# Kernel optimization log

Measured on AMD Instinct MI355X. Metric: run time of the kernel, lower is better.

Reference implementation:

```python
import jax, jax.numpy as jnp
import numpy as np

B, L, C, H = 1, 256, 128, 4  # batch, seq len, c_z, n_heads
D = C // H                    # head_dim = 32


def setup_inputs() -> dict:
    key = jax.random.key(0)
    ks = jax.random.split(key, 8)
    w = lambda k, shape: jax.random.normal(k, shape, jnp.float32) * 0.02
    return {
        "pair": jax.random.normal(ks[0], (B, L, L, C), jnp.float32),
        "ln_g": jnp.ones((C,), jnp.float32),
        "ln_b": jnp.zeros((C,), jnp.float32),
        "Wq": w(ks[1], (C, C)),
        "Wk": w(ks[2], (C, C)),
        "Wv": w(ks[3], (C, C)),
        "Wbias": w(ks[4], (C, H)),
        "Wo": w(ks[5], (C, C)),
        "bo": jnp.zeros((C,), jnp.float32),
        "Wg": w(ks[6], (C, C)),
        "bg": jnp.zeros((C,), jnp.float32),
    }


def reference(pair, ln_g, ln_b, Wq, Wk, Wv, Wbias, Wo, bo, Wg, bg):
    # mode == 'starting': no transpose of pair
    # LayerNorm over c_z
    mu = jnp.mean(pair, axis=-1, keepdims=True)
    var = jnp.mean(jnp.square(pair - mu), axis=-1, keepdims=True)
    z = (pair - mu) * jax.lax.rsqrt(var + 1e-5) * ln_g + ln_b

    q = (z @ Wq).reshape(B, L, L, H, D)
    k = (z @ Wk).reshape(B, L, L, H, D)
    v = (z @ Wv).reshape(B, L, L, H, D)

    # logits: [B, H, i, j, k], scaled by 1/sqrt(head_dim)
    attn = jnp.einsum('bijhd,bikhd->bhijk', q, k) * (1.0 / np.sqrt(D).astype(np.float32))
    # pairwise additive bias: bias_proj(z) -> [B, L, L, H] -> [B, H, 1, j, k]
    bias = jnp.einsum('bjkc,ch->bhjk', z, Wbias)[:, :, None, :, :]
    attn = jax.nn.softmax(attn + bias, axis=-1)

    out = jnp.einsum('bhijk,bikhd->bijhd', attn, v).reshape(B, L, L, C)
    result = pair + jax.nn.sigmoid(pair @ Wg + bg) * (out @ Wo + bo)
    return result
```

## Files before the change

kernel.cpp:

```cpp
#include <hip/hip_runtime.h>
#include <cstdint>
#include <cstddef>

#define L_ 256
#define C_ 128
#define H_ 4
#define D_ 32
#define NP_ (L_ * L_)

typedef unsigned short u16;
typedef uint32_t u32;
typedef __attribute__((ext_vector_type(8))) short bf16x8;
typedef __attribute__((ext_vector_type(4))) float f32x4;

__device__ __forceinline__ float bflo(u32 u) { union { u32 i; float f; } v; v.i = u << 16; return v.f; }
__device__ __forceinline__ float bfhi(u32 u) { union { u32 i; float f; } v; v.i = u & 0xffff0000u; return v.f; }
__device__ __forceinline__ float b2f(u16 u) { union { u32 i; float f; } v; v.i = ((u32)u) << 16; return v.f; }
__device__ __forceinline__ u16 f2b(float f) {
    u32 x = __float_as_uint(f);
    return (u16)((x + 0x7fffu + ((x >> 16) & 1u)) >> 16);
}
__device__ __forceinline__ u32 pk2(float lo, float hi) {
    return ((u32)f2b(hi) << 16) | (u32)f2b(lo);
}
__device__ __forceinline__ bf16x8 pack8(float4 a, float4 b) {
    union { u32 u[4]; bf16x8 v; } r;
    r.u[0] = pk2(a.x, a.y); r.u[1] = pk2(a.z, a.w);
    r.u[2] = pk2(b.x, b.y); r.u[3] = pk2(b.z, b.w);
    return r.v;
}

__global__ __launch_bounds__(256) void k_prep(
    const float* __restrict__ Wq, const float* __restrict__ Wk, const float* __restrict__ Wv,
    const float* __restrict__ Wo, const float* __restrict__ Wg,
    const float* __restrict__ Wbias, u16* __restrict__ Wt, float* __restrict__ WbT)
{
    __shared__ float tile[64][65];
    const int b = blockIdx.x, t = threadIdx.x;
    if (b < 20) {
        const int mat = b >> 2, tl = b & 3, tr = tl >> 1, tc = tl & 1;
        const float* W = (mat == 0) ? Wq : (mat == 1) ? Wk : (mat == 2) ? Wv : (mat == 3) ? Wo : Wg;
        const float s = (mat == 0) ? 0.2550680544705824f : 1.f;
        const int rlo = t >> 6, col = t & 63;
        #pragma unroll
        for (int m = 0; m < 16; ++m) {
            int row = m * 4 + rlo;
            tile[row][col] = W[(size_t)(tr * 64 + row) * C_ + tc * 64 + col];
        }
        __syncthreads();
        #pragma unroll
        for (int m = 0; m < 16; ++m) {
            int n = tc * 64 + m * 4 + rlo;
            int c = tr * 64 + col;
            Wt[mat * 16384 + n * C_ + c] = f2b(tile[col][m * 4 + rlo] * s);
        }
    } else {
        #pragma unroll
        for (int m = 0; m < 2; ++m) {
            int idx = m * 256 + t;
            int h = idx >> 7, c = idx & 127;
            WbT[h * C_ + c] = Wbias[c * H_ + h] * 1.4426950408889634f;
        }
    }
}

__global__ __launch_bounds__(256) void k_lnmm(
    const float* __restrict__ pair, const float* __restrict__ ln_g, const float* __restrict__ ln_b,
    const u16* __restrict__ Wt, const float* __restrict__ WbT,
    u16* __restrict__ qh, u16* __restrict__ kh, u16* __restrict__ vh,
    u16* __restrict__ biasN)
{
    __shared__ u16 zsh[64][136];

    const int t  = threadIdx.x;
    const int p0 = blockIdx.x * 64;
    const int row = t >> 2, seg = t & 3;

    float4 xv[8];
    float sum = 0.f, ss = 0.f;
    #pragma unroll
    for (int i = 0; i < 8; ++i) {
        int c = (seg + 4 * i) * 4;
        float4 x = *(const float4*)(pair + (size_t)(p0 + row) * C_ + c);
        xv[i] = x;
        sum += x.x + x.y + x.z + x.w;
        ss  += x.x * x.x + x.y * x.y + x.z * x.z + x.w * x.w;
    }
    sum += __shfl_xor(sum, 1); sum += __shfl_xor(sum, 2);
    ss  += __shfl_xor(ss, 1);  ss  += __shfl_xor(ss, 2);
    float mu  = sum * (1.0f / C_);
    float var = ss * (1.0f / C_) - mu * mu;
    float rs  = rsqrtf(fmaxf(var, 0.f) + 1e-5f);

    #pragma unroll
    for (int i = 0; i < 8; ++i) {
        int c = (seg + 4 * i) * 4;
        float4 g4 = *(const float4*)(ln_g + c);
        float4 b4 = *(const float4*)(ln_b + c);
        float4 x  = xv[i];
        float z0 = (x.x - mu) * rs * g4.x + b4.x;
        float z1 = (x.y - mu) * rs * g4.y + b4.y;
        float z2 = (x.z - mu) * rs * g4.z + b4.z;
        float z3 = (x.w - mu) * rs * g4.w + b4.w;
        *(u32*)&zsh[row][c]     = pk2(z0, z1);
        *(u32*)&zsh[row][c + 2] = pk2(z2, z3);
    }
    __syncthreads();

    const int w    = t >> 6;
    const int l15  = t & 15;
    const int quad = (t >> 4) & 3;

    bf16x8 zf[4][4];
    #pragma unroll
    for (int jt = 0; jt < 4; ++jt)
        #pragma unroll
        for (int kc = 0; kc < 4; ++kc)
            zf[jt][kc] = *(const bf16x8*)&zsh[jt * 16 + l15][kc * 32 + quad * 8];

    #pragma unroll
    for (int k = 0; k < 6; ++k) {
        const int tt = w * 6 + k;
        const int mat = tt >> 3, mt = tt & 7;
        f32x4 acc0 = {0.f,0.f,0.f,0.f}, acc1 = acc0, acc2 = acc0, acc3 = acc0;
        #pragma unroll
        for (int kc = 0; kc < 4; ++kc) {
            bf16x8 af = *(const bf16x8*)(Wt + (size_t)tt * 2048 + (size_t)l15 * 128 + kc * 32 + quad * 8);
            acc0 = __builtin_amdgcn_mfma_f32_16x16x32_bf16(af, zf[0][kc], acc0, 0, 0, 0);
            acc1 = __builtin_amdgcn_mfma_f32_16x16x32_bf16(af, zf[1][kc], acc1, 0, 0, 0);
            acc2 = __builtin_amdgcn_mfma_f32_16x16x32_bf16(af, zf[2][kc], acc2, 0, 0, 0);
            acc3 = __builtin_amdgcn_mfma_f32_16x16x32_bf16(af, zf[3][kc], acc3, 0, 0, 0);
        }
        u16* dst = (mat == 0) ? qh : (mat == 1) ? kh : vh;
        const int hh = mt >> 1;
        const int cb = (mt & 1) * 16 + quad * 4;
        f32x4 accs[4] = {acc0, acc1, acc2, acc3};
        #pragma unroll
        for (int jt = 0; jt < 4; ++jt) {
            const int p = p0 + jt * 16 + l15;
            *(uint2*)(dst + ((size_t)hh * NP_ + p) * D_ + cb) =
                make_uint2(pk2(accs[jt][0], accs[jt][1]), pk2(accs[jt][2], accs[jt][3]));
        }
    }

    {
        float a = 0.f;
        #pragma unroll
        for (int c8 = 0; c8 < C_; c8 += 8) {
            uint4 zz = *(const uint4*)&zsh[row][c8];
            float4 wb0 = *(const float4*)(WbT + seg * C_ + c8);
            float4 wb1 = *(const float4*)(WbT + seg * C_ + c8 + 4);
            a += bflo(zz.x) * wb0.x + bfhi(zz.x) * wb0.y
               + bflo(zz.y) * wb0.z + bfhi(zz.y) * wb0.w
               + bflo(zz.z) * wb1.x + bfhi(zz.z) * wb1.y
               + bflo(zz.w) * wb1.z + bfhi(zz.w) * wb1.w;
        }
        const int p = p0 + row;
        biasN[(size_t)seg * NP_ + p] = f2b(a);
    }
}

__global__ __launch_bounds__(1024)
__attribute__((amdgpu_waves_per_eu(4, 4)))
void k_ao(
    const u16* __restrict__ qh, const u16* __restrict__ kh, const u16* __restrict__ vh,
    const u16* __restrict__ biasN, const float* __restrict__ pair,
    const u16* __restrict__ Wt, const float* __restrict__ bo,
    const float* __restrict__ bg, float* __restrict__ out)
{
    __shared__ __align__(16) char shA[88064];
    __shared__ u16 ao_sh[256 * 136];

    u16* Vsh = reinterpret_cast<u16*>(shA);
    auto Psh = reinterpret_cast<u16(*)[16][40]>(shA + 67584);

    const int t = threadIdx.x;
    const int i = blockIdx.x;
    const int wave = t >> 6;
    const int h    = wave >> 2;
    const int ww   = wave & 3;
    const int l15  = t & 15;
    const int quad = (t >> 4) & 3;
    const int jbase = ww * 64;

    const u16* Kg = kh + ((size_t)h * NP_ + i * L_) * D_;
    const u16* Qg = qh + ((size_t)h * NP_ + i * L_) * D_;

    #pragma unroll
    for (int jj = 0; jj < 4; ++jj) {
        int idx = t + jj * 1024;
        int hs = idx >> 10, rem = idx & 1023;
        int r = rem >> 2, sg = rem & 3;
        const u16* Vg = vh + ((size_t)hs * NP_ + i * L_) * D_;
        union { uint4 q; u16 s[8]; } u;
        u.q = *(const uint4*)(Vg + r * D_ + sg * 8);
        #pragma unroll
        for (int m = 0; m < 8; ++m) Vsh[hs * 8448 + (sg * 8 + m) * 264 + r] = u.s[m];
    }

    bf16x8 qf[4];
    #pragma unroll
    for (int jt = 0; jt < 4; ++jt)
        qf[jt] = *(const bf16x8*)(Qg + (size_t)(jbase + jt * 16 + l15) * D_ + quad * 8);

    __syncthreads();

    const f32x4 z4 = {0.f, 0.f, 0.f, 0.f};
    f32x4 oacc[4][2], osum[4];
    #pragma unroll
    for (int jt = 0; jt < 4; ++jt) {
        oacc[jt][0] = z4; oacc[jt][1] = z4; osum[jt] = z4;
    }

    bf16x8 onesb;
    { union { u32 u[4]; bf16x8 v; } ob;
      ob.u[0] = ob.u[1] = ob.u[2] = ob.u[3] = 0x3F803F80u; onesb = ob.v; }

    const u16* bN = biasN + (size_t)h * NP_;
    const u16* Vs = Vsh + h * 8448;

    bf16x8 kb0 = *(const bf16x8*)(Kg + (size_t)l15 * D_ + quad * 8);
    bf16x8 kb1 = *(const bf16x8*)(Kg + (size_t)(16 + l15) * D_ + quad * 8);

    for (int kc = 0; kc < 8; ++kc) {
        bf16x8 nb0, nb1;
        if (kc < 7) {
            nb0 = *(const bf16x8*)(Kg + (size_t)((kc + 1) * 32 + l15) * D_ + quad * 8);
            nb1 = *(const bf16x8*)(Kg + (size_t)((kc + 1) * 32 + 16 + l15) * D_ + quad * 8);
        }
        bf16x8 vb0 = *(const bf16x8*)&Vs[l15 * 264 + kc * 32 + quad * 8];
        bf16x8 vb1 = *(const bf16x8*)&Vs[(16 + l15) * 264 + kc * 32 + quad * 8];

        #pragma unroll
        for (int jt = 0; jt < 4; ++jt) {
            f32x4 s0 = __builtin_amdgcn_mfma_f32_16x16x32_bf16(kb0, qf[jt], z4, 0, 0, 0);
            f32x4 s1 = __builtin_amdgcn_mfma_f32_16x16x32_bf16(kb1, qf[jt], z4, 0, 0, 0);

            const u16* bp = bN + (size_t)(jbase + jt * 16 + l15) * L_ + kc * 32 + quad * 4;
            uint2 bv0 = *(const uint2*)bp;
            uint2 bv1 = *(const uint2*)(bp + 16);
            const u16* b0p = (const u16*)&bv0;
            const u16* b1p = (const u16*)&bv1;

            float e0[4], e1[4];
            #pragma unroll
            for (int r = 0; r < 4; ++r) {
                e0[r] = __builtin_amdgcn_exp2f(s0[r] + b2f(b0p[r]));
                e1[r] = __builtin_amdgcn_exp2f(s1[r] + b2f(b1p[r]));
            }

            u32 w0, w1, w2, w3;
            asm("v_cvt_pk_bf16_f32 %0, %1, %2" : "=v"(w0) : "v"(e0[0]), "v"(e0[1]));
            asm("v_cvt_pk_bf16_f32 %0, %1, %2" : "=v"(w1) : "v"(e0[2]), "v"(e0[3]));
            asm("v_cvt_pk_bf16_f32 %0, %1, %2" : "=v"(w2) : "v"(e1[0]), "v"(e1[1]));
            asm("v_cvt_pk_bf16_f32 %0, %1, %2" : "=v"(w3) : "v"(e1[2]), "v"(e1[3]));
            *(uint2*)&Psh[wave][l15][quad * 4]      = make_uint2(w0, w1);
            *(uint2*)&Psh[wave][l15][16 + quad * 4] = make_uint2(w2, w3);

            bf16x8 pa = *(const bf16x8*)&Psh[wave][l15][quad * 8];
            oacc[jt][0] = __builtin_amdgcn_mfma_f32_16x16x32_bf16(pa, vb0,   oacc[jt][0], 0, 0, 0);
            oacc[jt][1] = __builtin_amdgcn_mfma_f32_16x16x32_bf16(pa, vb1,   oacc[jt][1], 0, 0, 0);
            osum[jt]    = __builtin_amdgcn_mfma_f32_16x16x32_bf16(pa, onesb, osum[jt],    0, 0, 0);
        }
        kb0 = nb0; kb1 = nb1;
    }

    #pragma unroll
    for (int jt = 0; jt < 4; ++jt) {
        #pragma unroll
        for (int r = 0; r < 4; ++r) {
            float rn = 1.f / osum[jt][r];
            int prow = jbase + jt * 16 + quad * 4 + r;
            ao_sh[prow * 136 + h * 32 + l15]      = f2b(oacc[jt][0][r] * rn);
            ao_sh[prow * 136 + h * 32 + 16 + l15] = f2b(oacc[jt][1][r] * rn);
        }
    }

    __syncthreads();

    u16* WoSh = reinterpret_cast<u16*>(shA);
    u16* WgSh = WoSh + 128 * 136;
    {
        const u16* WoT = Wt + 3 * 16384;
        const u16* WgT = Wt + 4 * 16384;
        #pragma unroll
        for (int m = 0; m < 2; ++m) {
            int idx = t + m * 1024;
            int rw = idx >> 4, cl = (idx & 15) * 8;
            *(uint4*)&WoSh[rw * 136 + cl] = *(const uint4*)(WoT + rw * 128 + cl);
            *(uint4*)&WgSh[rw * 136 + cl] = *(const uint4*)(WgT + rw * 128 + cl);
        }
    }
    __syncthreads();

    const int prow_l = wave * 16 + l15;
    const int pg     = i * L_ + prow_l;

    bf16x8 aof[4], pf[4];
    #pragma unroll
    for (int kc = 0; kc < 4; ++kc) {
        aof[kc] = *(const bf16x8*)&ao_sh[prow_l * 136 + kc * 32 + quad * 8];
        const float* pp = pair + (size_t)pg * C_ + kc * 32 + quad * 8;
        pf[kc] = pack8(*(const float4*)pp, *(const float4*)(pp + 4));
    }

    #pragma unroll
    for (int nt = 0; nt < 8; ++nt) {
        f32x4 accO = {0.f,0.f,0.f,0.f}, accG = accO;
        #pragma unroll
        for (int kc = 0; kc < 4; ++kc) {
            bf16x8 awo = *(const bf16x8*)&WoSh[(nt * 16 + l15) * 136 + kc * 32 + quad * 8];
            bf16x8 awg = *(const bf16x8*)&WgSh[(nt * 16 + l15) * 136 + kc * 32 + quad * 8];
            accO = __builtin_amdgcn_mfma_f32_16x16x32_bf16(awo, aof[kc], accO, 0, 0, 0);
            accG = __builtin_amdgcn_mfma_f32_16x16x32_bf16(awg, pf[kc],  accG, 0, 0, 0);
        }
        const int ch = nt * 16 + quad * 4;
        float4 bo4 = *(const float4*)(bo + ch);
        float4 bg4 = *(const float4*)(bg + ch);
        float4 pr  = *(const float4*)(pair + (size_t)pg * C_ + ch);
        float4 r;
        r.x = pr.x + (1.f / (1.f + __expf(-(accG[0] + bg4.x)))) * (accO[0] + bo4.x);
        r.y = pr.y + (1.f / (1.f + __expf(-(accG[1] + bg4.y)))) * (accO[1] + bo4.y);
        r.z = pr.z + (1.f / (1.f + __expf(-(accG[2] + bg4.z)))) * (accO[2] + bo4.z);
        r.w = pr.w + (1.f / (1.f + __expf(-(accG[3] + bg4.w)))) * (accO[3] + bo4.w);
        *(float4*)(out + (size_t)pg * C_ + ch) = r;
    }
}

extern "C" void kernel_launch(void* const* d_in, const int* in_sizes, int n_in,
                              void* d_out, int out_size, void* d_ws, size_t ws_size,
                              hipStream_t stream) {
    const float* pair  = (const float*)d_in[0];
    const float* ln_g  = (const float*)d_in[1];
    const float* ln_b  = (const float*)d_in[2];
    const float* Wq    = (const float*)d_in[3];
    const float* Wk    = (const float*)d_in[4];
    const float* Wv    = (const float*)d_in[5];
    const float* Wbias = (const float*)d_in[6];
    const float* Wo    = (const float*)d_in[7];
    const float* bo    = (const float*)d_in[8];
    const float* Wg    = (const float*)d_in[9];
    const float* bg    = (const float*)d_in[10];
    float* out = (float*)d_out;

    u16* biasN = (u16*)d_ws;
    u16* qh = biasN + (size_t)H_ * NP_;
    u16* kh = qh + (size_t)NP_ * C_;
    u16* vh = kh + (size_t)NP_ * C_;
    u16* Wt = vh + (size_t)NP_ * C_;
    float* WbT = (float*)(Wt + 5 * 16384);

    k_prep<<<21, 256, 0, stream>>>(Wq, Wk, Wv, Wo, Wg, Wbias, Wt, WbT);
    k_lnmm<<<NP_ / 64, 256, 0, stream>>>(pair, ln_g, ln_b, Wt, WbT, qh, kh, vh, biasN);
    k_ao<<<L_, 1024, 0, stream>>>(qh, kh, vh, biasN, pair, Wt, bo, bg, out);
}
```

Before: 193.9 us.

## Process four 32-row chunks per LN+QKV block with register prefetch of next chunk

The LayerNorm+QKV projection kernel now handles 128 positions per block in four 32-row chunks, prefetching the next chunk's pair rows into registers while the current chunk's MFMA projection runs. The grid is halved to 512 blocks and the LDS tile shrinks to 32 rows. The aim is to overlap global loads with compute and to amortize weight fragment reads, at the cost of fewer blocks, extra barriers per chunk, and only half the threads doing the bias projection.

After: 205.5 us. 6.0% more time.

```diff
diff --git a/kernel.cpp b/kernel.cpp
--- a/kernel.cpp
+++ b/kernel.cpp
@@ -70,93 +70,115 @@
     u16* __restrict__ qh, u16* __restrict__ kh, u16* __restrict__ vh,
     u16* __restrict__ biasN)
 {
-    __shared__ u16 zsh[64][136];
-
-    const int t  = threadIdx.x;
-    const int p0 = blockIdx.x * 64;
-    const int row = t >> 2, seg = t & 3;
-
-    float4 xv[8];
-    float sum = 0.f, ss = 0.f;
-    #pragma unroll
-    for (int i = 0; i < 8; ++i) {
-        int c = (seg + 4 * i) * 4;
-        float4 x = *(const float4*)(pair + (size_t)(p0 + row) * C_ + c);
-        xv[i] = x;
-        sum += x.x + x.y + x.z + x.w;
-        ss  += x.x * x.x + x.y * x.y + x.z * x.z + x.w * x.w;
-    }
-    sum += __shfl_xor(sum, 1); sum += __shfl_xor(sum, 2);
-    ss  += __shfl_xor(ss, 1);  ss  += __shfl_xor(ss, 2);
-    float mu  = sum * (1.0f / C_);
-    float var = ss * (1.0f / C_) - mu * mu;
-    float rs  = rsqrtf(fmaxf(var, 0.f) + 1e-5f);
-
-    #pragma unroll
-    for (int i = 0; i < 8; ++i) {
-        int c = (seg + 4 * i) * 4;
-        float4 g4 = *(const float4*)(ln_g + c);
-        float4 b4 = *(const float4*)(ln_b + c);
-        float4 x  = xv[i];
-        float z0 = (x.x - mu) * rs * g4.x + b4.x;
-        float z1 = (x.y - mu) * rs * g4.y + b4.y;
-        float z2 = (x.z - mu) * rs * g4.z + b4.z;
-        float z3 = (x.w - mu) * rs * g4.w + b4.w;
-        *(u32*)&zsh[row][c]     = pk2(z0, z1);
-        *(u32*)&zsh[row][c + 2] = pk2(z2, z3);
-    }
-    __syncthreads();
-
+    __shared__ u16 zsh[32][136];
+
+    const int t    = threadIdx.x;
+    const int p0   = blockIdx.x * 128;
+    const int row  = t >> 3, seg = t & 7;
     const int w    = t >> 6;
     const int l15  = t & 15;
     const int quad = (t >> 4) & 3;
 
-    bf16x8 zf[4][4];
-    #pragma unroll
-    for (int jt = 0; jt < 4; ++jt)
-        #pragma unroll
-        for (int kc = 0; kc < 4; ++kc)
-            zf[jt][kc] = *(const bf16x8*)&zsh[jt * 16 + l15][kc * 32 + quad * 8];
-
-    #pragma unroll
-    for (int k = 0; k < 6; ++k) {
-        const int tt = w * 6 + k;
-        const int mat = tt >> 3, mt = tt & 7;
-        f32x4 acc0 = {0.f,0.f,0.f,0.f}, acc1 = acc0, acc2 = acc0, acc3 = acc0;
-        #pragma unroll
-        for (int kc = 0; kc < 4; ++kc) {
-            bf16x8 af = *(const bf16x8*)(Wt + (size_t)tt * 2048 + (size_t)l15 * 128 + kc * 32 + quad * 8);
-            acc0 = __builtin_amdgcn_mfma_f32_16x16x32_bf16(af, zf[0][kc], acc0, 0, 0, 0);
-            acc1 = __builtin_amdgcn_mfma_f32_16x16x32_bf16(af, zf[1][kc], acc1, 0, 0, 0);
-            acc2 = __builtin_amdgcn_mfma_f32_16x16x32_bf16(af, zf[2][kc], acc2, 0, 0, 0);
-            acc3 = __builtin_amdgcn_mfma_f32_16x16x32_bf16(af, zf[3][kc], acc3, 0, 0, 0);
-        }
-        u16* dst = (mat == 0) ? qh : (mat == 1) ? kh : vh;
-        const int hh = mt >> 1;
-        const int cb = (mt & 1) * 16 + quad * 4;
-        f32x4 accs[4] = {acc0, acc1, acc2, acc3};
-        #pragma unroll
-        for (int jt = 0; jt < 4; ++jt) {
-            const int p = p0 + jt * 16 + l15;
-            *(uint2*)(dst + ((size_t)hh * NP_ + p) * D_ + cb) =
-                make_uint2(pk2(accs[jt][0], accs[jt][1]), pk2(accs[jt][2], accs[jt][3]));
-        }
-    }
-
-    {
-        float a = 0.f;
-        #pragma unroll
-        for (int c8 = 0; c8 < C_; c8 += 8) {
-            uint4 zz = *(const uint4*)&zsh[row][c8];
-            float4 wb0 = *(const float4*)(WbT + seg * C_ + c8);
-            float4 wb1 = *(const float4*)(WbT + seg * C_ + c8 + 4);
-            a += bflo(zz.x) * wb0.x + bfhi(zz.x) * wb0.y
-               + bflo(zz.y) * wb0.z + bfhi(zz.y) * wb0.w
-               + bflo(zz.z) * wb1.x + bfhi(zz.z) * wb1.y
-               + bflo(zz.w) * wb1.z + bfhi(zz.w) * wb1.w;
-        }
-        const int p = p0 + row;
-        biasN[(size_t)seg * NP_ + p] = f2b(a);
+    float4 xv[4], xvN[4];
+
+    #pragma unroll
+    for (int i = 0; i < 4; ++i) {
+        int c = (seg + 8 * i) * 4;
+        xv[i] = *(const float4*)(pair + (size_t)(p0 + row) * C_ + c);
+    }
+
+    #pragma unroll
+    for (int chk = 0; chk < 4; ++chk) {
+        const int pc = p0 + chk * 32;
+
+        float sum = 0.f, ss = 0.f;
+        #pragma unroll
+        for (int i = 0; i < 4; ++i) {
+            float4 x = xv[i];
+            sum += x.x + x.y + x.z + x.w;
+            ss  += x.x * x.x + x.y * x.y + x.z * x.z + x.w * x.w;
+        }
+        sum += __shfl_xor(sum, 1); sum += __shfl_xor(sum, 2); sum += __shfl_xor(sum, 4);
+        ss  += __shfl_xor(ss, 1);  ss  += __shfl_xor(ss, 2);  ss  += __shfl_xor(ss, 4);
+        float mu  = sum * (1.0f / C_);
+        float var = ss * (1.0f / C_) - mu * mu;
+        float rs  = rsqrtf(fmaxf(var, 0.f) + 1e-5f);
+
+        #pragma unroll
+        for (int i = 0; i < 4; ++i) {
+            int c = (seg + 8 * i) * 4;
+            float4 g4 = *(const float4*)(ln_g + c);
+            float4 b4 = *(const float4*)(ln_b + c);
+            float4 x  = xv[i];
+            float z0 = (x.x - mu) * rs * g4.x + b4.x;
+            float z1 = (x.y - mu) * rs * g4.y + b4.y;
+            float z2 = (x.z - mu) * rs * g4.z + b4.z;
+            float z3 = (x.w - mu) * rs * g4.w + b4.w;
+            *(u32*)&zsh[row][c]     = pk2(z0, z1);
+            *(u32*)&zsh[row][c + 2] = pk2(z2, z3);
+        }
+        __syncthreads();
+
+        if (chk < 3) {
+            #pragma unroll
+            for (int i = 0; i < 4; ++i) {
+                int c = (seg + 8 * i) * 4;
+                xvN[i] = *(const float4*)(pair + (size_t)(pc + 32 + row) * C_ + c);
+            }
+        }
+
+        bf16x8 zf[2][4];
+        #pragma unroll
+        for (int jt = 0; jt < 2; ++jt)
+            #pragma unroll
+            for (int kc = 0; kc < 4; ++kc)
+                zf[jt][kc] = *(const bf16x8*)&zsh[jt * 16 + l15][kc * 32 + quad * 8];
+
+        #pragma unroll
+        for (int k = 0; k < 6; ++k) {
+            const int tt = w * 6 + k;
+            const int mat = tt >> 3, mt = tt & 7;
+            f32x4 acc0 = {0.f,0.f,0.f,0.f}, acc1 = acc0;
+            #pragma unroll
+            for (int kc = 0; kc < 4; ++kc) {
+                bf16x8 af = *(const bf16x8*)(Wt + (size_t)tt * 2048 + (size_t)l15 * 128 + kc * 32 + quad * 8);
+                acc0 = __builtin_amdgcn_mfma_f32_16x16x32_bf16(af, zf[0][kc], acc0, 0, 0, 0);
+                acc1 = __builtin_amdgcn_mfma_f32_16x16x32_bf16(af, zf[1][kc], acc1, 0, 0, 0);
+            }
+            u16* dst = (mat == 0) ? qh : (mat == 1) ? kh : vh;
+            const int hh = mt >> 1;
+            const int cb = (mt & 1) * 16 + quad * 4;
+            f32x4 accs[2] = {acc0, acc1};
+            #pragma unroll
+            for (int jt = 0; jt < 2; ++jt) {
+                const int p = pc + jt * 16 + l15;
+                *(uint2*)(dst + ((size_t)hh * NP_ + p) * D_ + cb) =
+                    make_uint2(pk2(accs[jt][0], accs[jt][1]), pk2(accs[jt][2], accs[jt][3]));
+            }
+        }
+
+        if (t < 128) {
+            const int row2 = t >> 2, seg2 = t & 3;
+            float a = 0.f;
+            #pragma unroll
+            for (int c8 = 0; c8 < C_; c8 += 8) {
+                uint4 zz = *(const uint4*)&zsh[row2][c8];
+                float4 wb0 = *(const float4*)(WbT + seg2 * C_ + c8);
+                float4 wb1 = *(const float4*)(WbT + seg2 * C_ + c8 + 4);
+                a += bflo(zz.x) * wb0.x + bfhi(zz.x) * wb0.y
+                   + bflo(zz.y) * wb0.z + bfhi(zz.y) * wb0.w
+                   + bflo(zz.z) * wb1.x + bfhi(zz.z) * wb1.y
+                   + bflo(zz.w) * wb1.z + bfhi(zz.w) * wb1.w;
+            }
+            const int p = pc + row2;
+            biasN[(size_t)seg2 * NP_ + p] = f2b(a);
+        }
+        __syncthreads();
+
+        if (chk < 3) {
+            #pragma unroll
+            for (int i = 0; i < 4; ++i) xv[i] = xvN[i];
+        }
     }
 }
 
@@ -351,6 +373,6 @@
     float* WbT = (float*)(Wt + 5 * 16384);
 
     k_prep<<<21, 256, 0, stream>>>(Wq, Wk, Wv, Wo, Wg, Wbias, Wt, WbT);
-    k_lnmm<<<NP_ / 64, 256, 0, stream>>>(pair, ln_g, ln_b, Wt, WbT, qh, kh, vh, biasN);
+    k_lnmm<<<NP_ / 128, 256, 0, stream>>>(pair, ln_g, ln_b, Wt, WbT, qh, kh, vh, biasN);
     k_ao<<<L_, 1024, 0, stream>>>(qh, kh, vh, biasN, pair, Wt, bo, bg, out);
 }
```
